# Optimization experiments

Hardware: AMD Instinct MI355X
Metric: run time of the kernel (lower is better)

The kernel has to match this reference:

```python
import jax, jax.numpy as jnp
import numpy as np

N_NODES = 50000
N_EDGES = 800000
N_GRAPHS = 64
NEG_SLOPE = 0.2  # PyG GATv2Conv default negative_slope
LN_EPS = 1e-5


def gatv2(x, src, dst, Wl, bl, Wr, br, att, bias, heads, out_ch, concat):
    """Faithful eval-mode PyG GATv2Conv: x_l=lin_l(x) (source), x_r=lin_r(x) (target),
    e = att . leaky_relu(x_l[src] + x_r[dst]), segment-softmax over dst, scatter-add."""
    N = x.shape[0]
    H, C = heads, out_ch
    xl = (x @ Wl + bl).reshape(N, H, C)
    xr = (x @ Wr + br).reshape(N, H, C)
    e = jax.nn.leaky_relu(xl[src] + xr[dst], NEG_SLOPE)        # [E, H, C]
    logits = jnp.einsum('ehc,hc->eh', e, att)                  # [E, H]
    m = jax.ops.segment_max(logits, dst, num_segments=N)       # every node has a self-loop
    ex = jnp.exp(logits - m[dst])
    denom = jax.ops.segment_sum(ex, dst, num_segments=N)
    alpha = ex / (denom[dst] + 1e-16)                          # [E, H]
    out = jax.ops.segment_sum(xl[src] * alpha[..., None], dst, num_segments=N)  # [N, H, C]
    out = out.reshape(N, H * C) if concat else out.mean(axis=1)
    return out + bias


def setup_inputs() -> dict:
    key = jax.random.key(0)
    ks = jax.random.split(key, 32)

    def g(i, shape):  # glorot-ish
        scale = np.sqrt(2.0 / (shape[0] + shape[-1]))
        return (jax.random.normal(ks[i], shape, jnp.float32) * scale)

    inp = {
        'x': jax.random.normal(ks[0], (N_NODES, 4), jnp.float32),
        'edge_index': jax.random.randint(ks[1], (2, N_EDGES), 0, N_NODES, dtype=jnp.int64),
        'batch': jnp.sort(jax.random.randint(ks[2], (N_NODES,), 0, N_GRAPHS, dtype=jnp.int64)),
        # conv1: 4 -> 64, heads=4, concat -> 256
        'W1l': g(3, (4, 256)), 'b1l': jnp.zeros((256,), jnp.float32),
        'W1r': g(4, (4, 256)), 'b1r': jnp.zeros((256,), jnp.float32),
        'a1': g(5, (4, 64)), 'c1b': jnp.zeros((256,), jnp.float32),
        # conv2: 256 -> 64, heads=2, concat -> 128
        'W2l': g(6, (256, 128)), 'b2l': jnp.zeros((128,), jnp.float32),
        'W2r': g(7, (256, 128)), 'b2r': jnp.zeros((128,), jnp.float32),
        'a2': g(8, (2, 64)), 'c2b': jnp.zeros((128,), jnp.float32),
        # conv3: 128 -> 256, heads=1, concat=False -> 256
        'W3l': g(9, (128, 256)), 'b3l': jnp.zeros((256,), jnp.float32),
        'W3r': g(10, (128, 256)), 'b3r': jnp.zeros((256,), jnp.float32),
        'a3': g(11, (1, 256)), 'c3b': jnp.zeros((256,), jnp.float32),
        # enhancer MLP + LayerNorm
        'We1': g(12, (256, 512)), 'be1': jnp.zeros((512,), jnp.float32),
        'We2': g(13, (512, 256)), 'be2': jnp.zeros((256,), jnp.float32),
        'lng': jnp.ones((256,), jnp.float32), 'lnb': jnp.zeros((256,), jnp.float32),
    }
    return inp


def reference(x, edge_index, batch,
              W1l, b1l, W1r, b1r, a1, c1b,
              W2l, b2l, W2r, b2r, a2, c2b,
              W3l, b3l, W3r, b3r, a3, c3b,
              We1, be1, We2, be2, lng, lnb):
    N = x.shape[0]
    loop = jnp.arange(N, dtype=edge_index.dtype)  # add_self_loops=True (PyG default)
    src = jnp.concatenate([edge_index[0], loop])
    dst = jnp.concatenate([edge_index[1], loop])

    h = jax.nn.relu(gatv2(x, src, dst, W1l, b1l, W1r, b1r, a1, c1b, 4, 64, True))
    h = jax.nn.relu(gatv2(h, src, dst, W2l, b2l, W2r, b2r, a2, c2b, 2, 64, True))
    h = gatv2(h, src, dst, W3l, b3l, W3r, b3r, a3, c3b, 1, 256, False)

    # global mean pool per graph
    sums = jax.ops.segment_sum(h, batch, num_segments=N_GRAPHS)          # [G, 256]
    cnt = jax.ops.segment_sum(jnp.ones((N, 1), h.dtype), batch, num_segments=N_GRAPHS)
    pooled = sums / jnp.maximum(cnt, 1.0)

    # enhancer (dropout off in eval): Linear -> ReLU -> Linear -> LayerNorm
    z = jax.nn.relu(pooled @ We1 + be1) @ We2 + be2
    mu = z.mean(axis=-1, keepdims=True)
    var = z.var(axis=-1, keepdims=True)
    return (z - mu) / jnp.sqrt(var + LN_EPS) * lng + lnb
```

## Files before the change

### kernel.cpp

```cpp
#include <hip/hip_runtime.h>
#include <hip/hip_bf16.h>
#include <math.h>

#define NN 50000
#define NE0 800000
#define ETOT (NE0 + NN)
#define NG 64
#define SCAN_BLKS ((NN + 63) / 64)
#define DMAX_THR 8.0f

typedef __bf16 bf16x8 __attribute__((ext_vector_type(8)));
typedef float  f32x4  __attribute__((ext_vector_type(4)));
typedef unsigned short us8 __attribute__((ext_vector_type(8)));

__device__ __forceinline__ float bf2f(unsigned short u) {
    return __uint_as_float(((unsigned)u) << 16);
}
__device__ __forceinline__ unsigned short f2bf(float f) {
    unsigned u = __float_as_uint(f);
    return (unsigned short)((u + 0x7FFFu + ((u >> 16) & 1u)) >> 16);
}

__device__ __forceinline__ void edge_sd(const int* __restrict__ ei, int e, int& s, int& d) {
    if (e < NE0) { s = ei[e]; d = ei[NE0 + e]; }
    else { s = e - NE0; d = s; }
}

__global__ __launch_bounds__(256)
void hist_dst(const int* __restrict__ ei, int* __restrict__ deg) {
    int e = blockIdx.x * blockDim.x + threadIdx.x;
    if (e >= ETOT) return;
    int s, d; edge_sd(ei, e, s, d); (void)s;
    atomicAdd(&deg[d], 1);
}

__global__ __launch_bounds__(64)
void scan1(const int* __restrict__ deg, int* __restrict__ psum) {
    int i = blockIdx.x * 64 + threadIdx.x;
    int v = (i < NN) ? deg[i] : 0;
#pragma unroll
    for (int off = 1; off < 64; off <<= 1) {
        int t = __shfl_up(v, off);
        if ((int)threadIdx.x >= off) v += t;
    }
    if (threadIdx.x == 63) psum[blockIdx.x] = v;
}

__global__ __launch_bounds__(1024)
void scan2(int* __restrict__ psum) {
    __shared__ int sm[1024];
    int t = threadIdx.x;
    sm[t] = (t < SCAN_BLKS) ? psum[t] : 0;
    __syncthreads();
    for (int off = 1; off < 1024; off <<= 1) {
        int v = (t >= off) ? sm[t - off] : 0;
        __syncthreads();
        sm[t] += v;
        __syncthreads();
    }
    if (t < SCAN_BLKS) psum[t] = (t == 0) ? 0 : sm[t - 1];
}

__global__ __launch_bounds__(64)
void scan3(const int* __restrict__ deg, const int* __restrict__ psum,
           int* __restrict__ rowptr) {
    int i = blockIdx.x * 64 + threadIdx.x;
    int v = (i < NN) ? deg[i] : 0;
    int inc = v;
#pragma unroll
    for (int off = 1; off < 64; off <<= 1) {
        int t = __shfl_up(inc, off);
        if ((int)threadIdx.x >= off) inc += t;
    }
    int excl = inc - v + psum[blockIdx.x];
    if (i < NN) rowptr[i] = excl;
    if (i == NN - 1) rowptr[NN] = excl + v;
}

__global__ __launch_bounds__(256)
void scatter_csr(const int* __restrict__ ei, int* __restrict__ cursor,
                 int* __restrict__ col) {
    int e = blockIdx.x * blockDim.x + threadIdx.x;
    if (e >= ETOT) return;
    int s, d; edge_sd(ei, e, s, d);
    int pos = atomicAdd(&cursor[d], 1);
    col[pos] = s;
}

__device__ __forceinline__ void wfrag_one(const float* W, unsigned short* Wf,
                                          int r, int KB, int NOUT) {
    int j = r & 7;
    int l = (r >> 3) & 63;
    int rest = r >> 9;
    int kb = rest % KB, t = rest / KB;
    int k = kb * 32 + (l >> 4) * 8 + j;
    int colj = t * 16 + (l & 15);
    Wf[r] = f2bf(W[(size_t)k * NOUT + colj]);
}
__global__ __launch_bounds__(256)
void wfrag_all(const float* __restrict__ W2l, const float* __restrict__ W2r,
               const float* __restrict__ W3l, const float* __restrict__ W3r,
               unsigned short* __restrict__ Wf2l, unsigned short* __restrict__ Wf2r,
               unsigned short* __restrict__ Wf3l, unsigned short* __restrict__ Wf3r) {
    int tid = blockIdx.x * 256 + threadIdx.x;
    int seg = tid >> 15;
    int r = tid & 32767;
    if (seg == 0)      wfrag_one(W2l, Wf2l, r, 8, 128);
    else if (seg == 1) wfrag_one(W2r, Wf2r, r, 8, 128);
    else if (seg == 2) wfrag_one(W3l, Wf3l, r, 4, 256);
    else               wfrag_one(W3r, Wf3r, r, 4, 256);
}

__global__ __launch_bounds__(256)
void blr_prep(const float* __restrict__ X, const float* __restrict__ W1r,
              const float* __restrict__ b1r, const float* __restrict__ b1l,
              float* __restrict__ out) {
    int j = blockIdx.x * 64 + (threadIdx.x & 63);
    int row0 = (blockIdx.y * 4 + (threadIdx.x >> 6)) * 8;
    float w0 = W1r[j], w1 = W1r[256 + j], w2 = W1r[512 + j], w3 = W1r[768 + j];
    float bj = b1r[j] + b1l[j];
#pragma unroll
    for (int r = 0; r < 8; ++r) {
        int row = row0 + r;
        if (row >= NN) break;
        float4 xv = *reinterpret_cast<const float4*>(X + (size_t)row * 4);
        out[(size_t)row * 256 + j] =
            fmaf(xv.x, w0, fmaf(xv.y, w1, fmaf(xv.z, w2, fmaf(xv.w, w3, bj))));
    }
}

__global__ __launch_bounds__(256)
void gat1_fused(const float* __restrict__ x,
                const int* __restrict__ rowptr, const int* __restrict__ col,
                const float* __restrict__ BLR,
                const float* __restrict__ W1l, const float* __restrict__ b1l,
                const float* __restrict__ a1, const float* __restrict__ c1b,
                unsigned short* __restrict__ out) {
    int lane = threadIdx.x & 63;
    int node = (blockIdx.x * blockDim.x + threadIdx.x) >> 6;
    if (node >= NN) return;
    int ch0 = lane * 4;

    float wl[4][4];
#pragma unroll
    for (int k = 0; k < 4; ++k) {
        float4 l4 = *reinterpret_cast<const float4*>(W1l + k * 256 + ch0);
        wl[k][0] = l4.x; wl[k][1] = l4.y; wl[k][2] = l4.z; wl[k][3] = l4.w;
    }
    float4 av  = *reinterpret_cast<const float4*>(a1 + ch0);
    float ar[4] = { av.x, av.y, av.z, av.w };
    float4 blv = *reinterpret_cast<const float4*>(b1l + ch0);
    float4 cbv = *reinterpret_cast<const float4*>(c1b + ch0);
    float obias[4] = { blv.x + cbv.x, blv.y + cbv.y, blv.z + cbv.z, blv.w + cbv.w };

    const float4* x4 = reinterpret_cast<const float4*>(x);

    float4 blrv = *reinterpret_cast<const float4*>(BLR + (size_t)node * 256 + ch0);
    float blr[4] = { blrv.x, blrv.y, blrv.z, blrv.w };

    float m = -INFINITY, l = 0.f;
    float ax = 0.f, ay = 0.f, az = 0.f, aw = 0.f;

    int beg = rowptr[node], end = rowptr[node + 1];
    int idx = beg;
    for (; idx + 3 < end; idx += 4) {
        float4 v[4];
        float dd[4];
#pragma unroll
        for (int q = 0; q < 4; ++q) v[q] = x4[col[idx + q]];
#pragma unroll
        for (int q = 0; q < 4; ++q) {
            float d = 0.f;
#pragma unroll
            for (int p = 0; p < 4; ++p) {
                float u = fmaf(v[q].x, wl[0][p], fmaf(v[q].y, wl[1][p],
                          fmaf(v[q].z, wl[2][p], fmaf(v[q].w, wl[3][p], blr[p]))));
                u = u > 0.f ? u : 0.2f * u;
                d = fmaf(u, ar[p], d);
            }
            dd[q] = d;
        }
#pragma unroll
        for (int off = 8; off >= 1; off >>= 1) {
#pragma unroll
            for (int q = 0; q < 4; ++q) dd[q] += __shfl_xor(dd[q], off);
        }
        float pmax = fmaxf(fmaxf(dd[0], dd[1]), fmaxf(dd[2], dd[3]));
        if (pmax > m + DMAX_THR) {
            float sc = __expf(m - pmax);
            l *= sc; ax *= sc; ay *= sc; az *= sc; aw *= sc;
            m = pmax;
        }
        float p0 = __expf(dd[0] - m), p1 = __expf(dd[1] - m);
        float p2 = __expf(dd[2] - m), p3 = __expf(dd[3] - m);
        l += (p0 + p1) + (p2 + p3);
        ax += fmaf(p0, v[0].x, p1 * v[1].x) + fmaf(p2, v[2].x, p3 * v[3].x);
        ay += fmaf(p0, v[0].y, p1 * v[1].y) + fmaf(p2, v[2].y, p3 * v[3].y);
        az += fmaf(p0, v[0].z, p1 * v[1].z) + fmaf(p2, v[2].z, p3 * v[3].z);
        aw += fmaf(p0, v[0].w, p1 * v[1].w) + fmaf(p2, v[2].w, p3 * v[3].w);
    }
    for (; idx < end; ++idx) {
        float4 v0 = x4[col[idx]];
        float d0 = 0.f;
#pragma unroll
        for (int p = 0; p < 4; ++p) {
            float u0 = fmaf(v0.x, wl[0][p], fmaf(v0.y, wl[1][p],
                       fmaf(v0.z, wl[2][p], fmaf(v0.w, wl[3][p], blr[p]))));
            u0 = u0 > 0.f ? u0 : 0.2f * u0;
            d0 = fmaf(u0, ar[p], d0);
        }
#pragma unroll
        for (int off = 8; off >= 1; off >>= 1) d0 += __shfl_xor(d0, off);
        if (d0 > m + DMAX_THR) {
            float sc = __expf(m - d0);
            l *= sc; ax *= sc; ay *= sc; az *= sc; aw *= sc;
            m = d0;
        }
        float p0 = __expf(d0 - m);
        l += p0;
        ax = fmaf(p0, v0.x, ax);
        ay = fmaf(p0, v0.y, ay);
        az = fmaf(p0, v0.z, az);
        aw = fmaf(p0, v0.w, aw);
    }
    float inv = 1.f / (l + 1e-16f);
    unsigned short o[4];
#pragma unroll
    for (int p = 0; p < 4; ++p) {
        float v = fmaf(ax, wl[0][p], fmaf(ay, wl[1][p],
                  fmaf(az, wl[2][p], aw * wl[3][p]))) * inv + obias[p];
        o[p] = f2bf(fmaxf(v, 0.f));
    }
    *reinterpret_cast<ushort4*>(out + (size_t)node * 256 + ch0) =
        make_ushort4(o[0], o[1], o[2], o[3]);
}

template<int KIN, int NOUT>
__global__ __launch_bounds__(256)
void gemm_mfma2(const unsigned short* __restrict__ X,
                const unsigned short* __restrict__ WfL, const float* __restrict__ bL,
                unsigned short* __restrict__ outL,
                const unsigned short* __restrict__ WfR, const float* __restrict__ bR,
                unsigned short* __restrict__ outR) {
    constexpr int KB = KIN / 32, NT = NOUT / 16;
    int lane = threadIdx.x & 63;
    int wv = threadIdx.x >> 6;
    int row0 = blockIdx.x * 64 + wv * 16;
    int r16 = lane & 15, kg = lane >> 4;

    int arow = row0 + r16; if (arow >= NN) arow = NN - 1;
    const unsigned short* xrow = X + (size_t)arow * KIN + kg * 8;
    bf16x8 af[KB];
#pragma unroll
    for (int kb = 0; kb < KB; ++kb)
        af[kb] = *reinterpret_cast<const bf16x8*>(xrow + kb * 32);

    const unsigned short* Wf[2] = { WfL, WfR };
    const float* bb[2] = { bL, bR };
    unsigned short* oo[2] = { outL, outR };

#pragma unroll
    for (int w = 0; w < 2; ++w) {
        const bf16x8* wbase = reinterpret_cast<const bf16x8*>(Wf[w]) + lane;
        const float* bw = bb[w];
        unsigned short* ow = oo[w];
#pragma unroll 1
        for (int t = 0; t < NT; ++t) {
            f32x4 acc = {0.f, 0.f, 0.f, 0.f};
            const bf16x8* wp = wbase + (size_t)t * KB * 64;
#pragma unroll
            for (int kb = 0; kb < KB; ++kb)
                acc = __builtin_amdgcn_mfma_f32_16x16x32_bf16(af[kb], wp[kb * 64], acc, 0, 0, 0);
            float bv = bw[t * 16 + r16];
#pragma unroll
            for (int rg = 0; rg < 4; ++rg) {
                int row = row0 + kg * 4 + rg;
                if (row < NN)
                    ow[(size_t)row * NOUT + t * 16 + r16] = f2bf(acc[rg] + bv);
            }
        }
    }
}

__global__ __launch_bounds__(256)
void gat2_fused(const unsigned short* __restrict__ xl, const unsigned short* __restrict__ xr,
                const int* __restrict__ rowptr, const int* __restrict__ col,
                const float* __restrict__ att, const float* __restrict__ bias,
                unsigned short* __restrict__ out) {
    constexpr int HC = 128, CPL = 2, GRP = 32;
    int lane = threadIdx.x & 63;
    int node = (blockIdx.x * blockDim.x + threadIdx.x) >> 6;
    if (node >= NN) return;
    int ch0 = lane * CPL;

    float areg[CPL], breg[CPL];
#pragma unroll
    for (int p = 0; p < CPL; ++p) { areg[p] = att[ch0 + p]; breg[p] = bias[ch0 + p]; }

    float xrv[CPL];
    {
        ushort2 u = *reinterpret_cast<const ushort2*>(xr + (size_t)node * HC + ch0);
        xrv[0] = bf2f(u.x); xrv[1] = bf2f(u.y);
    }
    float m = -INFINITY, l = 0.f, acc[CPL];
#pragma unroll
    for (int p = 0; p < CPL; ++p) acc[p] = 0.f;

    int beg = rowptr[node], end = rowptr[node + 1];
    int idx = beg;
    for (; idx + 3 < end; idx += 4) {
        float a[4][CPL];
        float dd[4];
#pragma unroll
        for (int q = 0; q < 4; ++q) {
            int s = col[idx + q];
            ushort2 u = *reinterpret_cast<const ushort2*>(xl + (size_t)s * HC + ch0);
            a[q][0] = bf2f(u.x); a[q][1] = bf2f(u.y);
        }
#pragma unroll
        for (int q = 0; q < 4; ++q) {
            float d = 0.f;
#pragma unroll
            for (int p = 0; p < CPL; ++p) {
                float v = a[q][p] + xrv[p];
                v = v > 0.f ? v : 0.2f * v;
                d = fmaf(v, areg[p], d);
            }
            dd[q] = d;
        }
#pragma unroll
        for (int off = GRP >> 1; off >= 1; off >>= 1) {
#pragma unroll
            for (int q = 0; q < 4; ++q) dd[q] += __shfl_xor(dd[q], off);
        }
        float pmax = fmaxf(fmaxf(dd[0], dd[1]), fmaxf(dd[2], dd[3]));
        if (pmax > m + DMAX_THR) {
            float sc = __expf(m - pmax);
            l *= sc;
#pragma unroll
            for (int p = 0; p < CPL; ++p) acc[p] *= sc;
            m = pmax;
        }
        float p0 = __expf(dd[0] - m), p1 = __expf(dd[1] - m);
        float p2 = __expf(dd[2] - m), p3 = __expf(dd[3] - m);
        l += (p0 + p1) + (p2 + p3);
#pragma unroll
        for (int p = 0; p < CPL; ++p)
            acc[p] += fmaf(p0, a[0][p], p1 * a[1][p]) + fmaf(p2, a[2][p], p3 * a[3][p]);
    }
    for (; idx < end; ++idx) {
        int s0 = col[idx];
        float a0[CPL];
        ushort2 u0 = *reinterpret_cast<const ushort2*>(xl + (size_t)s0 * HC + ch0);
        a0[0] = bf2f(u0.x); a0[1] = bf2f(u0.y);
        float d0 = 0.f;
#pragma unroll
        for (int p = 0; p < CPL; ++p) {
            float v0 = a0[p] + xrv[p];
            v0 = v0 > 0.f ? v0 : 0.2f * v0;
            d0 = fmaf(v0, areg[p], d0);
        }
#pragma unroll
        for (int off = GRP >> 1; off >= 1; off >>= 1) d0 += __shfl_xor(d0, off);
        if (d0 > m + DMAX_THR) {
            float sc = __expf(m - d0);
            l *= sc;
#pragma unroll
            for (int p = 0; p < CPL; ++p) acc[p] *= sc;
            m = d0;
        }
        float p0 = __expf(d0 - m);
        l += p0;
#pragma unroll
        for (int p = 0; p < CPL; ++p)
            acc[p] = fmaf(p0, a0[p], acc[p]);
    }
    float inv = 1.f / (l + 1e-16f);
    float o0 = fmaxf(acc[0] * inv + breg[0], 0.f);
    float o1 = fmaxf(acc[1] * inv + breg[1], 0.f);
    *reinterpret_cast<ushort2*>(out + (size_t)node * HC + ch0) =
        make_ushort2(f2bf(o0), f2bf(o1));
}

__global__ __launch_bounds__(256)
void gat3_fused(const unsigned short* __restrict__ xl, const unsigned short* __restrict__ xr,
                const int* __restrict__ rowptr, const int* __restrict__ col,
                const float* __restrict__ att, const float* __restrict__ bias,
                float* __restrict__ out) {
    int lane = threadIdx.x & 63;
    int half = lane >> 5;
    int node = (blockIdx.x * blockDim.x + threadIdx.x) >> 6;
    if (node >= NN) return;
    int ch0 = (lane & 31) * 8;

    float areg[8], xrv[8];
    {
        us8 ua = *reinterpret_cast<const us8*>(att + 0 + ch0), ux;
        (void)ua;
    }
#pragma unroll
    for (int p = 0; p < 8; ++p) areg[p] = att[ch0 + p];
    {
        us8 u = *reinterpret_cast<const us8*>(xr + (size_t)node * 256 + ch0);
#pragma unroll
        for (int p = 0; p < 8; ++p) xrv[p] = bf2f(u[p]);
    }

    float m = -INFINITY, l = 0.f, acc[8];
#pragma unroll
    for (int p = 0; p < 8; ++p) acc[p] = 0.f;

    int beg = rowptr[node], end = rowptr[node + 1];
    int n = end - beg;
    int nh = (n + 1) >> 1;
    int myBeg = beg + (half ? nh : 0);
    int myEnd = half ? end : beg + nh;

    int idx = myBeg;
    for (; idx + 1 < myEnd; idx += 2) {
        int s0 = col[idx], s1 = col[idx + 1];
        float a0[8], a1[8];
        {
            us8 u0 = *reinterpret_cast<const us8*>(xl + (size_t)s0 * 256 + ch0);
            us8 u1 = *reinterpret_cast<const us8*>(xl + (size_t)s1 * 256 + ch0);
#pragma unroll
            for (int p = 0; p < 8; ++p) { a0[p] = bf2f(u0[p]); a1[p] = bf2f(u1[p]); }
        }
        float d0 = 0.f, d1 = 0.f;
#pragma unroll
        for (int p = 0; p < 8; ++p) {
            float v0 = a0[p] + xrv[p];
            float v1 = a1[p] + xrv[p];
            v0 = v0 > 0.f ? v0 : 0.2f * v0;
            v1 = v1 > 0.f ? v1 : 0.2f * v1;
            d0 = fmaf(v0, areg[p], d0);
            d1 = fmaf(v1, areg[p], d1);
        }
#pragma unroll
        for (int off = 16; off >= 1; off >>= 1) {
            d0 += __shfl_xor(d0, off);
            d1 += __shfl_xor(d1, off);
        }
        float pmax = fmaxf(d0, d1);
        if (pmax > m + DMAX_THR) {
            float sc = __expf(m - pmax);
            l *= sc;
#pragma unroll
            for (int p = 0; p < 8; ++p) acc[p] *= sc;
            m = pmax;
        }
        float p0 = __expf(d0 - m), p1 = __expf(d1 - m);
        l += p0 + p1;
#pragma unroll
        for (int p = 0; p < 8; ++p)
            acc[p] += fmaf(p0, a0[p], p1 * a1[p]);
    }
    if (idx < myEnd) {
        int s0 = col[idx];
        float a0[8];
        us8 u0 = *reinterpret_cast<const us8*>(xl + (size_t)s0 * 256 + ch0);
#pragma unroll
        for (int p = 0; p < 8; ++p) a0[p] = bf2f(u0[p]);
        float d0 = 0.f;
#pragma unroll
        for (int p = 0; p < 8; ++p) {
            float v0 = a0[p] + xrv[p];
            v0 = v0 > 0.f ? v0 : 0.2f * v0;
            d0 = fmaf(v0, areg[p], d0);
        }
#pragma unroll
        for (int off = 16; off >= 1; off >>= 1) d0 += __shfl_xor(d0, off);
        if (d0 > m + DMAX_THR) {
            float sc = __expf(m - d0);
            l *= sc;
#pragma unroll
            for (int p = 0; p < 8; ++p) acc[p] *= sc;
            m = d0;
        }
        float p0 = __expf(d0 - m);
        l += p0;
#pragma unroll
        for (int p = 0; p < 8; ++p)
            acc[p] = fmaf(p0, a0[p], acc[p]);
    }

    float mo = __shfl_xor(m, 32);
    float lo = __shfl_xor(l, 32);
    float M = fmaxf(m, mo);
    float sA = __expf(m - M), sB = __expf(mo - M);
    float lsum = l * sA + lo * sB;
    float inv = 1.f / (lsum + 1e-16f);
    float o[8];
#pragma unroll
    for (int p = 0; p < 8; ++p) {
        float ao = __shfl_xor(acc[p], 32);
        o[p] = (acc[p] * sA + ao * sB) * inv + bias[ch0 + p];
    }
    if (half == 0) {
        *reinterpret_cast<float4*>(out + (size_t)node * 256 + ch0) =
            make_float4(o[0], o[1], o[2], o[3]);
        *reinterpret_cast<float4*>(out + (size_t)node * 256 + ch0 + 4) =
            make_float4(o[4], o[5], o[6], o[7]);
    }
}

__global__ __launch_bounds__(64)
void graph_bounds(const int* __restrict__ batch, float* __restrict__ cnt) {
    int g = threadIdx.x;
    if (g >= NG) return;
    int lo = 0, hi = NN;
    while (lo < hi) { int mid = (lo + hi) >> 1; if (batch[mid] < g) lo = mid + 1; else hi = mid; }
    int lo2 = lo, hi2 = NN;
    while (lo2 < hi2) { int mid = (lo2 + hi2) >> 1; if (batch[mid] < g + 1) lo2 = mid + 1; else hi2 = mid; }
    cnt[g] = (float)(lo2 - lo);
}

__global__ __launch_bounds__(256)
void pool_sum(const float* __restrict__ h, const int* __restrict__ batch,
              float* pooled) {
    __shared__ int gb[32];
    int c = threadIdx.x;
    int n0 = blockIdx.x * 32;
    int n1 = min(n0 + 32, NN);
    int cnt = n1 - n0;
    if (c < cnt) gb[c] = batch[n0 + c];
    __syncthreads();
    if (gb[0] == gb[cnt - 1]) {
        float acc = 0.f;
#pragma unroll 4
        for (int i = 0; i < cnt; ++i) acc += h[(size_t)(n0 + i) * 256 + c];
        atomicAdd(&pooled[gb[0] * 256 + c], acc);
    } else {
        int cur = gb[0]; float acc = 0.f;
        for (int i = 0; i < cnt; ++i) {
            int g = gb[i];
            if (g != cur) { atomicAdd(&pooled[cur * 256 + c], acc); acc = 0.f; cur = g; }
            acc += h[(size_t)(n0 + i) * 256 + c];
        }
        atomicAdd(&pooled[cur * 256 + c], acc);
    }
}

__global__ __launch_bounds__(256)
void mlp_ln(const float* __restrict__ pooled, const float* __restrict__ cnt,
            const float* __restrict__ We1, const float* __restrict__ be1,
            const float* __restrict__ We2, const float* __restrict__ be2,
            const float* __restrict__ lng, const float* __restrict__ lnb,
            float* __restrict__ out) {
    __shared__ float p[256];
    __shared__ float t[512];
    __shared__ float red[8];
    int g = blockIdx.x, tid = threadIdx.x;
    p[tid] = pooled[g * 256 + tid] / fmaxf(cnt[g], 1.0f);
    __syncthreads();
    for (int jj = tid; jj < 512; jj += 256) {
        float s = be1[jj];
        for (int k = 0; k < 256; ++k) s = fmaf(p[k], We1[(size_t)k * 512 + jj], s);
        t[jj] = fmaxf(s, 0.f);
    }
    __syncthreads();
    float z = be2[tid];
    for (int k = 0; k < 512; ++k) z = fmaf(t[k], We2[(size_t)k * 256 + tid], z);
    float sv = z, sq = z * z;
#pragma unroll
    for (int off = 32; off >= 1; off >>= 1) {
        sv += __shfl_xor(sv, off);
        sq += __shfl_xor(sq, off);
    }
    int wv = tid >> 6;
    if ((tid & 63) == 0) { red[wv] = sv; red[4 + wv] = sq; }
    __syncthreads();
    float tot = red[0] + red[1] + red[2] + red[3];
    float totq = red[4] + red[5] + red[6] + red[7];
    float mu = tot * (1.f / 256.f);
    float var = totq * (1.f / 256.f) - mu * mu;
    float r = rsqrtf(var + 1e-5f);
    out[g * 256 + tid] = (z - mu) * r * lng[tid] + lnb[tid];
}

extern "C" void kernel_launch(void* const* d_in, const int* in_sizes, int n_in,
                              void* d_out, int out_size, void* d_ws, size_t ws_size,
                              hipStream_t stream) {
    const float* x   = (const float*)d_in[0];
    const int*   ei  = (const int*)d_in[1];
    const int*   bat = (const int*)d_in[2];
    const float *W1l = (const float*)d_in[3], *b1l = (const float*)d_in[4];
    const float *W1r = (const float*)d_in[5], *b1r = (const float*)d_in[6];
    const float *a1  = (const float*)d_in[7], *c1b = (const float*)d_in[8];
    const float *W2l = (const float*)d_in[9],  *b2l = (const float*)d_in[10];
    const float *W2r = (const float*)d_in[11], *b2r = (const float*)d_in[12];
    const float *a2  = (const float*)d_in[13], *c2b = (const float*)d_in[14];
    const float *W3l = (const float*)d_in[15], *b3l = (const float*)d_in[16];
    const float *W3r = (const float*)d_in[17], *b3r = (const float*)d_in[18];
    const float *a3  = (const float*)d_in[19], *c3b = (const float*)d_in[20];
    const float *We1 = (const float*)d_in[21], *be1 = (const float*)d_in[22];
    const float *We2 = (const float*)d_in[23], *be2 = (const float*)d_in[24];
    const float *lng = (const float*)d_in[25], *lnb = (const float*)d_in[26];

    char* base = (char*)d_ws;
    size_t off = 0;
    auto nxt = [&](size_t bytes) { char* p = base + off; off = (off + bytes + 255) & ~(size_t)255; return p; };
    unsigned short* Abuf = (unsigned short*)nxt((size_t)NN * 256 * 2);
    unsigned short* Bbuf = (unsigned short*)nxt((size_t)NN * 256 * 2);
    unsigned short* Hb16 = (unsigned short*)nxt((size_t)NN * 256 * 2);
    float* Hb32 = (float*)nxt((size_t)NN * 256 * 4);
    float* BLR  = (float*)nxt((size_t)NN * 256 * 4);
    int* deg    = (int*)nxt(NN * 4);
    int* rowptr = (int*)nxt((NN + 1) * 4);
    int* cursor = (int*)nxt(NN * 4);
    int* colv   = (int*)nxt((size_t)ETOT * 4);
    int* psum   = (int*)nxt(1024 * 4);
    float* POOL = (float*)nxt(NG * 256 * 4);
    float* CNT  = (float*)nxt(NG * 4);
    unsigned short* Wf2l = (unsigned short*)nxt(256 * 128 * 2);
    unsigned short* Wf2r = (unsigned short*)nxt(256 * 128 * 2);
    unsigned short* Wf3l = (unsigned short*)nxt(128 * 256 * 2);
    unsigned short* Wf3r = (unsigned short*)nxt(128 * 256 * 2);

    const int GEMM_BLKS = (NN + 63) / 64;
    const int NB_NODE = (NN + 3) / 4;

    hipMemsetAsync(deg, 0, NN * sizeof(int), stream);
    hist_dst<<<(ETOT + 255) / 256, 256, 0, stream>>>(ei, deg);
    scan1<<<SCAN_BLKS, 64, 0, stream>>>(deg, psum);
    scan2<<<1, 1024, 0, stream>>>(psum);
    scan3<<<SCAN_BLKS, 64, 0, stream>>>(deg, psum, rowptr);
    hipMemcpyAsync(cursor, rowptr, NN * sizeof(int), hipMemcpyDeviceToDevice, stream);
    scatter_csr<<<(ETOT + 255) / 256, 256, 0, stream>>>(ei, cursor, colv);

    wfrag_all<<<(4 * 32768) / 256, 256, 0, stream>>>(W2l, W2r, W3l, W3r, Wf2l, Wf2r, Wf3l, Wf3r);
    {
        dim3 g(4, (NN + 31) / 32);
        blr_prep<<<g, 256, 0, stream>>>(x, W1r, b1r, b1l, BLR);
    }

    gat1_fused<<<NB_NODE, 256, 0, stream>>>(x, rowptr, colv, BLR, W1l, b1l, a1, c1b, Hb16);

    gemm_mfma2<256, 128><<<GEMM_BLKS, 256, 0, stream>>>(Hb16, Wf2l, b2l, Abuf, Wf2r, b2r, Bbuf);
    gat2_fused<<<NB_NODE, 256, 0, stream>>>(Abuf, Bbuf, rowptr, colv, a2, c2b, Hb16);

    gemm_mfma2<128, 256><<<GEMM_BLKS, 256, 0, stream>>>(Hb16, Wf3l, b3l, Abuf, Wf3r, b3r, Bbuf);
    gat3_fused<<<NB_NODE, 256, 0, stream>>>(Abuf, Bbuf, rowptr, colv, a3, c3b, Hb32);

    hipMemsetAsync(POOL, 0, (size_t)NG * 256 * 4, stream);
    graph_bounds<<<1, 64, 0, stream>>>(bat, CNT);
    pool_sum<<<(NN + 31) / 32, 256, 0, stream>>>(Hb32, bat, POOL);
    mlp_ln<<<NG, 256, 0, stream>>>(POOL, CNT, We1, be1, We2, be2, lng, lnb, (float*)d_out);
}
```

Measured before the change: 472.7 us.

## Switch intermediates to fp16 with packed-half math, split gat2 edges across half-waves

Intermediate activations and weight fragments change from bf16 to fp16, and the GEMMs use the f16 MFMA. The gat2/gat3 edge loops compute the leaky-relu and attention dot with packed-half add/max and fdot2 instead of scalar fp32. gat2 now splits each node's edges between two half-waves with 4 channels per lane and merges their softmax states at the end. The cursor copy is folded into scan3 and the pool memset into graph_bounds to remove two launches, at the cost of fp16 range risk and reduced logit precision.

```diff
diff --git a/kernel.cpp b/kernel.cpp
--- a/kernel.cpp
+++ b/kernel.cpp
@@ -9,16 +9,13 @@
 #define SCAN_BLKS ((NN + 63) / 64)
 #define DMAX_THR 8.0f
 
-typedef __bf16 bf16x8 __attribute__((ext_vector_type(8)));
-typedef float  f32x4  __attribute__((ext_vector_type(4)));
-typedef unsigned short us8 __attribute__((ext_vector_type(8)));
-
-__device__ __forceinline__ float bf2f(unsigned short u) {
-    return __uint_as_float(((unsigned)u) << 16);
-}
-__device__ __forceinline__ unsigned short f2bf(float f) {
-    unsigned u = __float_as_uint(f);
-    return (unsigned short)((u + 0x7FFFu + ((u >> 16) & 1u)) >> 16);
+typedef _Float16 h2 __attribute__((ext_vector_type(2)));
+typedef _Float16 h8 __attribute__((ext_vector_type(8)));
+typedef float    f32x4 __attribute__((ext_vector_type(4)));
+
+__device__ __forceinline__ unsigned short f2h(float f) {
+    _Float16 h = (_Float16)f;
+    return __builtin_bit_cast(unsigned short, h);
 }
 
 __device__ __forceinline__ void edge_sd(const int* __restrict__ ei, int e, int& s, int& d) {
@@ -63,7 +60,7 @@
 
 __global__ __launch_bounds__(64)
 void scan3(const int* __restrict__ deg, const int* __restrict__ psum,
-           int* __restrict__ rowptr) {
+           int* __restrict__ rowptr, int* __restrict__ cursor) {
     int i = blockIdx.x * 64 + threadIdx.x;
     int v = (i < NN) ? deg[i] : 0;
     int inc = v;
@@ -73,7 +70,7 @@
         if ((int)threadIdx.x >= off) inc += t;
     }
     int excl = inc - v + psum[blockIdx.x];
-    if (i < NN) rowptr[i] = excl;
+    if (i < NN) { rowptr[i] = excl; cursor[i] = excl; }
     if (i == NN - 1) rowptr[NN] = excl + v;
 }
 
@@ -95,7 +92,7 @@
     int kb = rest % KB, t = rest / KB;
     int k = kb * 32 + (l >> 4) * 8 + j;
     int colj = t * 16 + (l & 15);
-    Wf[r] = f2bf(W[(size_t)k * NOUT + colj]);
+    Wf[r] = f2h(W[(size_t)k * NOUT + colj]);
 }
 __global__ __launch_bounds__(256)
 void wfrag_all(const float* __restrict__ W2l, const float* __restrict__ W2r,
@@ -229,7 +226,7 @@
     for (int p = 0; p < 4; ++p) {
         float v = fmaf(ax, wl[0][p], fmaf(ay, wl[1][p],
                   fmaf(az, wl[2][p], aw * wl[3][p]))) * inv + obias[p];
-        o[p] = f2bf(fmaxf(v, 0.f));
+        o[p] = f2h(fmaxf(v, 0.f));
     }
     *reinterpret_cast<ushort4*>(out + (size_t)node * 256 + ch0) =
         make_ushort4(o[0], o[1], o[2], o[3]);
@@ -250,10 +247,10 @@
 
     int arow = row0 + r16; if (arow >= NN) arow = NN - 1;
     const unsigned short* xrow = X + (size_t)arow * KIN + kg * 8;
-    bf16x8 af[KB];
+    h8 af[KB];
 #pragma unroll
     for (int kb = 0; kb < KB; ++kb)
-        af[kb] = *reinterpret_cast<const bf16x8*>(xrow + kb * 32);
+        af[kb] = *reinterpret_cast<const h8*>(xrow + kb * 32);
 
     const unsigned short* Wf[2] = { WfL, WfR };
     const float* bb[2] = { bL, bR };
@@ -261,22 +258,22 @@
 
 #pragma unroll
     for (int w = 0; w < 2; ++w) {
-        const bf16x8* wbase = reinterpret_cast<const bf16x8*>(Wf[w]) + lane;
+        const h8* wbase = reinterpret_cast<const h8*>(Wf[w]) + lane;
         const float* bw = bb[w];
         unsigned short* ow = oo[w];
 #pragma unroll 1
         for (int t = 0; t < NT; ++t) {
             f32x4 acc = {0.f, 0.f, 0.f, 0.f};
-            const bf16x8* wp = wbase + (size_t)t * KB * 64;
+            const h8* wp = wbase + (size_t)t * KB * 64;
 #pragma unroll
             for (int kb = 0; kb < KB; ++kb)
-                acc = __builtin_amdgcn_mfma_f32_16x16x32_bf16(af[kb], wp[kb * 64], acc, 0, 0, 0);
+                acc = __builtin_amdgcn_mfma_f32_16x16x32_f16(af[kb], wp[kb * 64], acc, 0, 0, 0);
             float bv = bw[t * 16 + r16];
 #pragma unroll
             for (int rg = 0; rg < 4; ++rg) {
                 int row = row0 + kg * 4 + rg;
                 if (row < NN)
-                    ow[(size_t)row * NOUT + t * 16 + r16] = f2bf(acc[rg] + bv);
+                    ow[(size_t)row * NOUT + t * 16 + r16] = f2h(acc[rg] + bv);
             }
         }
     }
@@ -287,99 +284,109 @@
                 const int* __restrict__ rowptr, const int* __restrict__ col,
                 const float* __restrict__ att, const float* __restrict__ bias,
                 unsigned short* __restrict__ out) {
-    constexpr int HC = 128, CPL = 2, GRP = 32;
+    constexpr int HC = 128;
     int lane = threadIdx.x & 63;
+    int half = lane >> 5;
+    int l32 = lane & 31;
     int node = (blockIdx.x * blockDim.x + threadIdx.x) >> 6;
     if (node >= NN) return;
-    int ch0 = lane * CPL;
-
-    float areg[CPL], breg[CPL];
-#pragma unroll
-    for (int p = 0; p < CPL; ++p) { areg[p] = att[ch0 + p]; breg[p] = bias[ch0 + p]; }
-
-    float xrv[CPL];
-    {
-        ushort2 u = *reinterpret_cast<const ushort2*>(xr + (size_t)node * HC + ch0);
-        xrv[0] = bf2f(u.x); xrv[1] = bf2f(u.y);
-    }
-    float m = -INFINITY, l = 0.f, acc[CPL];
-#pragma unroll
-    for (int p = 0; p < CPL; ++p) acc[p] = 0.f;
+    int ch0 = l32 * 4;
+
+    const h2 c02 = (h2){(_Float16)0.2f, (_Float16)0.2f};
+    h2 a2[2];
+#pragma unroll
+    for (int p = 0; p < 2; ++p)
+        a2[p] = (h2){(_Float16)att[ch0 + 2*p], (_Float16)att[ch0 + 2*p + 1]};
+    const h2* xrp = reinterpret_cast<const h2*>(xr + (size_t)node * HC + ch0);
+    h2 xr2[2] = { xrp[0], xrp[1] };
+
+    float m = -INFINITY, l = 0.f, acc[4] = {0.f, 0.f, 0.f, 0.f};
 
     int beg = rowptr[node], end = rowptr[node + 1];
-    int idx = beg;
-    for (; idx + 3 < end; idx += 4) {
-        float a[4][CPL];
-        float dd[4];
-#pragma unroll
-        for (int q = 0; q < 4; ++q) {
-            int s = col[idx + q];
-            ushort2 u = *reinterpret_cast<const ushort2*>(xl + (size_t)s * HC + ch0);
-            a[q][0] = bf2f(u.x); a[q][1] = bf2f(u.y);
-        }
-#pragma unroll
-        for (int q = 0; q < 4; ++q) {
-            float d = 0.f;
-#pragma unroll
-            for (int p = 0; p < CPL; ++p) {
-                float v = a[q][p] + xrv[p];
-                v = v > 0.f ? v : 0.2f * v;
-                d = fmaf(v, areg[p], d);
-            }
-            dd[q] = d;
-        }
-#pragma unroll
-        for (int off = GRP >> 1; off >= 1; off >>= 1) {
-#pragma unroll
-            for (int q = 0; q < 4; ++q) dd[q] += __shfl_xor(dd[q], off);
-        }
-        float pmax = fmaxf(fmaxf(dd[0], dd[1]), fmaxf(dd[2], dd[3]));
+    int n = end - beg;
+    int nh = (n + 1) >> 1;
+    int idx = beg + (half ? nh : 0);
+    int myEnd = half ? end : beg + nh;
+
+    for (; idx + 1 < myEnd; idx += 2) {
+        int s0 = col[idx], s1 = col[idx + 1];
+        const h2* p0 = reinterpret_cast<const h2*>(xl + (size_t)s0 * HC + ch0);
+        const h2* p1 = reinterpret_cast<const h2*>(xl + (size_t)s1 * HC + ch0);
+        h2 e0[2] = { p0[0], p0[1] };
+        h2 e1[2] = { p1[0], p1[1] };
+        float d0 = 0.f, d1 = 0.f;
+#pragma unroll
+        for (int p = 0; p < 2; ++p) {
+            h2 u0 = e0[p] + xr2[p];
+            h2 u1 = e1[p] + xr2[p];
+            u0 = __builtin_elementwise_max(u0, u0 * c02);
+            u1 = __builtin_elementwise_max(u1, u1 * c02);
+            d0 = __builtin_amdgcn_fdot2(u0, a2[p], d0, false);
+            d1 = __builtin_amdgcn_fdot2(u1, a2[p], d1, false);
+        }
+#pragma unroll
+        for (int off = 8; off >= 1; off >>= 1) {
+            d0 += __shfl_xor(d0, off);
+            d1 += __shfl_xor(d1, off);
+        }
+        float pmax = fmaxf(d0, d1);
         if (pmax > m + DMAX_THR) {
             float sc = __expf(m - pmax);
             l *= sc;
 #pragma unroll
-            for (int p = 0; p < CPL; ++p) acc[p] *= sc;
+            for (int p = 0; p < 4; ++p) acc[p] *= sc;
             m = pmax;
         }
-        float p0 = __expf(dd[0] - m), p1 = __expf(dd[1] - m);
-        float p2 = __expf(dd[2] - m), p3 = __expf(dd[3] - m);
-        l += (p0 + p1) + (p2 + p3);
-#pragma unroll
-        for (int p = 0; p < CPL; ++p)
-            acc[p] += fmaf(p0, a[0][p], p1 * a[1][p]) + fmaf(p2, a[2][p], p3 * a[3][p]);
-    }
-    for (; idx < end; ++idx) {
+        float pw0 = __expf(d0 - m), pw1 = __expf(d1 - m);
+        l += pw0 + pw1;
+#pragma unroll
+        for (int p = 0; p < 4; ++p)
+            acc[p] = fmaf(pw0, (float)e0[p >> 1][p & 1],
+                     fmaf(pw1, (float)e1[p >> 1][p & 1], acc[p]));
+    }
+    if (idx < myEnd) {
         int s0 = col[idx];
-        float a0[CPL];
-        ushort2 u0 = *reinterpret_cast<const ushort2*>(xl + (size_t)s0 * HC + ch0);
-        a0[0] = bf2f(u0.x); a0[1] = bf2f(u0.y);
+        const h2* p0 = reinterpret_cast<const h2*>(xl + (size_t)s0 * HC + ch0);
+        h2 e0[2] = { p0[0], p0[1] };
         float d0 = 0.f;
 #pragma unroll
-        for (int p = 0; p < CPL; ++p) {
-            float v0 = a0[p] + xrv[p];
-            v0 = v0 > 0.f ? v0 : 0.2f * v0;
-            d0 = fmaf(v0, areg[p], d0);
-        }
-#pragma unroll
-        for (int off = GRP >> 1; off >= 1; off >>= 1) d0 += __shfl_xor(d0, off);
+        for (int p = 0; p < 2; ++p) {
+            h2 u0 = e0[p] + xr2[p];
+            u0 = __builtin_elementwise_max(u0, u0 * c02);
+            d0 = __builtin_amdgcn_fdot2(u0, a2[p], d0, false);
+        }
+#pragma unroll
+        for (int off = 8; off >= 1; off >>= 1) d0 += __shfl_xor(d0, off);
         if (d0 > m + DMAX_THR) {
             float sc = __expf(m - d0);
             l *= sc;
 #pragma unroll
-            for (int p = 0; p < CPL; ++p) acc[p] *= sc;
+            for (int p = 0; p < 4; ++p) acc[p] *= sc;
             m = d0;
         }
-        float p0 = __expf(d0 - m);
-        l += p0;
-#pragma unroll
-        for (int p = 0; p < CPL; ++p)
-            acc[p] = fmaf(p0, a0[p], acc[p]);
-    }
-    float inv = 1.f / (l + 1e-16f);
-    float o0 = fmaxf(acc[0] * inv + breg[0], 0.f);
-    float o1 = fmaxf(acc[1] * inv + breg[1], 0.f);
-    *reinterpret_cast<ushort2*>(out + (size_t)node * HC + ch0) =
-        make_ushort2(f2bf(o0), f2bf(o1));
+        float pw0 = __expf(d0 - m);
+        l += pw0;
+#pragma unroll
+        for (int p = 0; p < 4; ++p)
+            acc[p] = fmaf(pw0, (float)e0[p >> 1][p & 1], acc[p]);
+    }
+
+    float mo = __shfl_xor(m, 32);
+    float lo = __shfl_xor(l, 32);
+    float M = fmaxf(m, mo);
+    float sA = __expf(m - M), sB = __expf(mo - M);
+    float lsum = l * sA + lo * sB;
+    float inv = 1.f / (lsum + 1e-16f);
+    unsigned short o[4];
+#pragma unroll
+    for (int p = 0; p < 4; ++p) {
+        float ao = __shfl_xor(acc[p], 32);
+        float v = (acc[p] * sA + ao * sB) * inv + bias[ch0 + p];
+        o[p] = f2h(fmaxf(v, 0.f));
+    }
+    if (half == 0)
+        *reinterpret_cast<ushort4*>(out + (size_t)node * HC + ch0) =
+            make_ushort4(o[0], o[1], o[2], o[3]);
 }
 
 __global__ __launch_bounds__(256)
@@ -393,18 +400,13 @@
     if (node >= NN) return;
     int ch0 = (lane & 31) * 8;
 
-    float areg[8], xrv[8];
-    {
-        us8 ua = *reinterpret_cast<const us8*>(att + 0 + ch0), ux;
-        (void)ua;
-    }
-#pragma unroll
-    for (int p = 0; p < 8; ++p) areg[p] = att[ch0 + p];
-    {
-        us8 u = *reinterpret_cast<const us8*>(xr + (size_t)node * 256 + ch0);
-#pragma unroll
-        for (int p = 0; p < 8; ++p) xrv[p] = bf2f(u[p]);
-    }
+    const h2 c02 = (h2){(_Float16)0.2f, (_Float16)0.2f};
+    h2 a2[4];
+#pragma unroll
+    for (int p = 0; p < 4; ++p)
+        a2[p] = (h2){(_Float16)att[ch0 + 2*p], (_Float16)att[ch0 + 2*p + 1]};
+    const h2* xrp = reinterpret_cast<const h2*>(xr + (size_t)node * 256 + ch0);
+    h2 xr2[4] = { xrp[0], xrp[1], xrp[2], xrp[3] };
 
     float m = -INFINITY, l = 0.f, acc[8];
 #pragma unroll
@@ -413,28 +415,24 @@
     int beg = rowptr[node], end = rowptr[node + 1];
     int n = end - beg;
     int nh = (n + 1) >> 1;
-    int myBeg = beg + (half ? nh : 0);
+    int idx = beg + (half ? nh : 0);
     int myEnd = half ? end : beg + nh;
 
-    int idx = myBeg;
     for (; idx + 1 < myEnd; idx += 2) {
         int s0 = col[idx], s1 = col[idx + 1];
-        float a0[8], a1[8];
-        {
-            us8 u0 = *reinterpret_cast<const us8*>(xl + (size_t)s0 * 256 + ch0);
-            us8 u1 = *reinterpret_cast<const us8*>(xl + (size_t)s1 * 256 + ch0);
-#pragma unroll
-            for (int p = 0; p < 8; ++p) { a0[p] = bf2f(u0[p]); a1[p] = bf2f(u1[p]); }
-        }
+        const h2* p0 = reinterpret_cast<const h2*>(xl + (size_t)s0 * 256 + ch0);
+        const h2* p1 = reinterpret_cast<const h2*>(xl + (size_t)s1 * 256 + ch0);
+        h2 e0[4] = { p0[0], p0[1], p0[2], p0[3] };
+        h2 e1[4] = { p1[0], p1[1], p1[2], p1[3] };
         float d0 = 0.f, d1 = 0.f;
 #pragma unroll
-        for (int p = 0; p < 8; ++p) {
-            float v0 = a0[p] + xrv[p];
-            float v1 = a1[p] + xrv[p];
-            v0 = v0 > 0.f ? v0 : 0.2f * v0;
-            v1 = v1 > 0.f ? v1 : 0.2f * v1;
-            d0 = fmaf(v0, areg[p], d0);
-            d1 = fmaf(v1, areg[p], d1);
+        for (int p = 0; p < 4; ++p) {
+            h2 u0 = e0[p] + xr2[p];
+            h2 u1 = e1[p] + xr2[p];
+            u0 = __builtin_elementwise_max(u0, u0 * c02);
+            u1 = __builtin_elementwise_max(u1, u1 * c02);
+            d0 = __builtin_amdgcn_fdot2(u0, a2[p], d0, false);
+            d1 = __builtin_amdgcn_fdot2(u1, a2[p], d1, false);
         }
 #pragma unroll
         for (int off = 16; off >= 1; off >>= 1) {
@@ -449,24 +447,23 @@
             for (int p = 0; p < 8; ++p) acc[p] *= sc;
             m = pmax;
         }
-        float p0 = __expf(d0 - m), p1 = __expf(d1 - m);
-        l += p0 + p1;
+        float pw0 = __expf(d0 - m), pw1 = __expf(d1 - m);
+        l += pw0 + pw1;
 #pragma unroll
         for (int p = 0; p < 8; ++p)
-            acc[p] += fmaf(p0, a0[p], p1 * a1[p]);
+            acc[p] = fmaf(pw0, (float)e0[p >> 1][p & 1],
+                     fmaf(pw1, (float)e1[p >> 1][p & 1], acc[p]));
     }
     if (idx < myEnd) {
         int s0 = col[idx];
-        float a0[8];
-        us8 u0 = *reinterpret_cast<const us8*>(xl + (size_t)s0 * 256 + ch0);
-#pragma unroll
-        for (int p = 0; p < 8; ++p) a0[p] = bf2f(u0[p]);
+        const h2* p0 = reinterpret_cast<const h2*>(xl + (size_t)s0 * 256 + ch0);
+        h2 e0[4] = { p0[0], p0[1], p0[2], p0[3] };
         float d0 = 0.f;
 #pragma unroll
-        for (int p = 0; p < 8; ++p) {
-            float v0 = a0[p] + xrv[p];
-            v0 = v0 > 0.f ? v0 : 0.2f * v0;
-            d0 = fmaf(v0, areg[p], d0);
+        for (int p = 0; p < 4; ++p) {
+            h2 u0 = e0[p] + xr2[p];
+            u0 = __builtin_elementwise_max(u0, u0 * c02);
+            d0 = __builtin_amdgcn_fdot2(u0, a2[p], d0, false);
         }
 #pragma unroll
         for (int off = 16; off >= 1; off >>= 1) d0 += __shfl_xor(d0, off);
@@ -477,11 +474,11 @@
             for (int p = 0; p < 8; ++p) acc[p] *= sc;
             m = d0;
         }
-        float p0 = __expf(d0 - m);
-        l += p0;
+        float pw0 = __expf(d0 - m);
+        l += pw0;
 #pragma unroll
         for (int p = 0; p < 8; ++p)
-            acc[p] = fmaf(p0, a0[p], acc[p]);
+            acc[p] = fmaf(pw0, (float)e0[p >> 1][p & 1], acc[p]);
     }
 
     float mo = __shfl_xor(m, 32);
@@ -504,15 +501,18 @@
     }
 }
 
-__global__ __launch_bounds__(64)
-void graph_bounds(const int* __restrict__ batch, float* __restrict__ cnt) {
-    int g = threadIdx.x;
-    if (g >= NG) return;
-    int lo = 0, hi = NN;
-    while (lo < hi) { int mid = (lo + hi) >> 1; if (batch[mid] < g) lo = mid + 1; else hi = mid; }
-    int lo2 = lo, hi2 = NN;
-    while (lo2 < hi2) { int mid = (lo2 + hi2) >> 1; if (batch[mid] < g + 1) lo2 = mid + 1; else hi2 = mid; }
-    cnt[g] = (float)(lo2 - lo);
+__global__ __launch_bounds__(256)
+void graph_bounds(const int* __restrict__ batch, float* __restrict__ cnt,
+                  float* __restrict__ pooled) {
+    int g = blockIdx.x, tid = threadIdx.x;
+    pooled[g * 256 + tid] = 0.f;
+    if (tid == 0) {
+        int lo = 0, hi = NN;
+        while (lo < hi) { int mid = (lo + hi) >> 1; if (batch[mid] < g) lo = mid + 1; else hi = mid; }
+        int lo2 = lo, hi2 = NN;
+        while (lo2 < hi2) { int mid = (lo2 + hi2) >> 1; if (batch[mid] < g + 1) lo2 = mid + 1; else hi2 = mid; }
+        cnt[g] = (float)(lo2 - lo);
+    }
 }
 
 __global__ __launch_bounds__(256)
@@ -624,8 +624,7 @@
     hist_dst<<<(ETOT + 255) / 256, 256, 0, stream>>>(ei, deg);
     scan1<<<SCAN_BLKS, 64, 0, stream>>>(deg, psum);
     scan2<<<1, 1024, 0, stream>>>(psum);
-    scan3<<<SCAN_BLKS, 64, 0, stream>>>(deg, psum, rowptr);
-    hipMemcpyAsync(cursor, rowptr, NN * sizeof(int), hipMemcpyDeviceToDevice, stream);
+    scan3<<<SCAN_BLKS, 64, 0, stream>>>(deg, psum, rowptr, cursor);
     scatter_csr<<<(ETOT + 255) / 256, 256, 0, stream>>>(ei, cursor, colv);
 
     wfrag_all<<<(4 * 32768) / 256, 256, 0, stream>>>(W2l, W2r, W3l, W3r, Wf2l, Wf2r, Wf3l, Wf3r);
@@ -642,8 +641,7 @@
     gemm_mfma2<128, 256><<<GEMM_BLKS, 256, 0, stream>>>(Hb16, Wf3l, b3l, Abuf, Wf3r, b3r, Bbuf);
     gat3_fused<<<NB_NODE, 256, 0, stream>>>(Abuf, Bbuf, rowptr, colv, a3, c3b, Hb32);
 
-    hipMemsetAsync(POOL, 0, (size_t)NG * 256 * 4, stream);
-    graph_bounds<<<1, 64, 0, stream>>>(bat, CNT);
+    graph_bounds<<<NG, 256, 0, stream>>>(bat, CNT, POOL);
     pool_sum<<<(NN + 31) / 32, 256, 0, stream>>>(Hb32, bat, POOL);
     mlp_ln<<<NG, 256, 0, stream>>>(POOL, CNT, We1, be1, We2, be2, lng, lnb, (float*)d_out);
 }
```

Result: faster. 441.1 us (-6.7%).
